# Optimization experiments

Measured on AMD Instinct MI355X. Metric: run time of the kernel, lower is better.

The kernel has to match this reference:

```python
import jax, jax.numpy as jnp
import numpy as np

DIM = 2048
N_HEADS = 16
N_KV_HEADS = 8
HEAD_DIM = DIM // N_HEADS  # 128
N_REP = N_HEADS // N_KV_HEADS
BATCH = 2
SEQ = 2048
CHUNK = 128  # chunked-parallel causal linear attention; SEQ % CHUNK == 0


def _make_freqs_cis(seq_len, head_dim, theta=10000.0):
    freqs = 1.0 / (theta ** (np.arange(0, head_dim, 2, dtype=np.float32) / head_dim))
    t = np.arange(seq_len, dtype=np.float32)
    ang = np.outer(t, freqs)  # [S, D/2]
    return jnp.asarray(np.stack([np.cos(ang), np.sin(ang)], axis=-1))  # [S, D/2, 2]


def setup_inputs() -> dict:
    key = jax.random.key(0)
    ks = jax.random.split(key, 5)
    x = jax.random.normal(ks[0], (BATCH, SEQ, DIM), dtype=jnp.float32)
    freqs_cis = _make_freqs_cis(SEQ, HEAD_DIM)
    s = 0.02
    wq = s * jax.random.normal(ks[1], (N_HEADS * HEAD_DIM, DIM), dtype=jnp.float32)
    wk = s * jax.random.normal(ks[2], (N_KV_HEADS * HEAD_DIM, DIM), dtype=jnp.float32)
    wv = s * jax.random.normal(ks[3], (N_KV_HEADS * HEAD_DIM, DIM), dtype=jnp.float32)
    wo = s * jax.random.normal(ks[4], (DIM, N_HEADS * HEAD_DIM), dtype=jnp.float32)
    return {"x": x, "freqs_cis": freqs_cis, "wq": wq, "wk": wk, "wv": wv, "wo": wo}


def _apply_rotary(x, freqs_cis):
    # x: [B, S, H, D]; freqs_cis: [S, D/2, 2] (cos, sin). Llama pairing: (x0,x1),(x2,x3),...
    B, S, H, D = x.shape
    xr = x.reshape(B, S, H, D // 2, 2)
    x0, x1 = xr[..., 0], xr[..., 1]
    c = freqs_cis[None, :, None, :, 0]
    s = freqs_cis[None, :, None, :, 1]
    o0 = x0 * c - x1 * s
    o1 = x0 * s + x1 * c
    return jnp.stack([o0, o1], axis=-1).reshape(B, S, H, D)


def _causal_linear_attention(q, k, v):
    # q, k, v: [B, H, S, D]; output_i = q_i @ sum_{j<=i} k_j^T v_j
    B, H, S, D = q.shape
    q = jax.nn.softmax(q * (D ** -0.5), axis=-1)  # softmax over feature dim
    k = jax.nn.softmax(k, axis=2)                 # softmax over sequence dim (as in source)
    Nc = S // CHUNK
    qc = q.reshape(B, H, Nc, CHUNK, D)
    kc = k.reshape(B, H, Nc, CHUNK, D)
    vc = v.reshape(B, H, Nc, CHUNK, D)
    # per-chunk KV outer-product sums: [B, H, Nc, D, D]
    kv = jnp.einsum('bhncd,bhnce->bhnde', kc, vc)
    cum = jnp.cumsum(kv, axis=2)
    cum_excl = jnp.concatenate([jnp.zeros_like(cum[:, :, :1]), cum[:, :, :-1]], axis=2)
    inter = jnp.einsum('bhncd,bhnde->bhnce', qc, cum_excl)
    scores = jnp.einsum('bhncd,bhnmd->bhncm', qc, kc)  # [B,H,Nc,C,C]
    mask = jnp.tril(jnp.ones((CHUNK, CHUNK), dtype=bool))
    scores = jnp.where(mask, scores, jnp.zeros((), dtype=scores.dtype))
    intra = jnp.einsum('bhncm,bhnme->bhnce', scores, vc)
    return (inter + intra).reshape(B, H, S, D)


def reference(x, freqs_cis, wq, wk, wv, wo):
    B, S, _ = x.shape
    xq = (x @ wq.T).reshape(B, S, N_HEADS, HEAD_DIM)
    xk = (x @ wk.T).reshape(B, S, N_KV_HEADS, HEAD_DIM)
    xv = (x @ wv.T).reshape(B, S, N_KV_HEADS, HEAD_DIM)
    xq = _apply_rotary(xq, freqs_cis)
    xk = _apply_rotary(xk, freqs_cis)
    # repeat_kv: each kv head repeated N_REP consecutive times
    keys = jnp.repeat(xk, N_REP, axis=2)
    values = jnp.repeat(xv, N_REP, axis=2)
    q = jnp.transpose(xq, (0, 2, 1, 3))
    k = jnp.transpose(keys, (0, 2, 1, 3))
    v = jnp.transpose(values, (0, 2, 1, 3))
    out = _causal_linear_attention(q, k, v)  # [B, H, S, D]
    out = jnp.transpose(out, (0, 2, 1, 3)).reshape(B, S, N_HEADS * HEAD_DIM)
    return out @ wo.T
```

## Files before the change

### kernel.cpp

```cpp
#include <hip/hip_runtime.h>
#include <math.h>

#define DIMV 2048
#define NHEAD 16
#define NKV 8
#define HD 128
#define BATCH 2
#define SEQ 2048
#define CHUNK 128
#define NCHUNK 16
#define MTOK 4096
#define KVD (NKV * HD)

typedef _Float16 half8_t __attribute__((ext_vector_type(8)));
typedef _Float16 half4_t __attribute__((ext_vector_type(4)));
typedef _Float16 half2_t __attribute__((ext_vector_type(2)));
typedef float f32x4 __attribute__((ext_vector_type(4)));

#define GLOBAL_AS __attribute__((address_space(1)))
#define LDS_AS __attribute__((address_space(3)))

__global__ __launch_bounds__(256) void cast_all(const float* __restrict__ x,
                                                const float* __restrict__ wq,
                                                const float* __restrict__ wk,
                                                const float* __restrict__ wv,
                                                const float* __restrict__ wo,
                                                _Float16* __restrict__ xh,
                                                _Float16* __restrict__ wqkvh,
                                                _Float16* __restrict__ woh) {
  long i = (long)(blockIdx.x * 256 + threadIdx.x) * 8;
  const float* src;
  _Float16* dst;
  long off;
  if (i < 8388608)        { src = x;  dst = xh;              off = 0; }
  else if (i < 12582912)  { src = wq; dst = wqkvh;           off = 8388608; }
  else if (i < 14680064)  { src = wk; dst = wqkvh + 4194304; off = 12582912; }
  else if (i < 16777216)  { src = wv; dst = wqkvh + 6291456; off = 14680064; }
  else                    { src = wo; dst = woh;             off = 16777216; }
  long e = i - off;
  float4 a = *(const float4*)&src[e];
  float4 b = *(const float4*)&src[e + 4];
  half8_t h = {(_Float16)a.x, (_Float16)a.y, (_Float16)a.z, (_Float16)a.w,
               (_Float16)b.x, (_Float16)b.y, (_Float16)b.z, (_Float16)b.w};
  *(half8_t*)&dst[e] = h;
}

__global__ __launch_bounds__(256) void transpose_fc(const float* __restrict__ fc,
                                                    float* __restrict__ fcT) {
  __shared__ float T[64][65];
  int s0 = blockIdx.x * 64, d0 = blockIdx.y * 64;
  int t = threadIdx.x;
  int r = t >> 4, c4 = (t & 15) * 4;
#pragma unroll
  for (int p = 0; p < 4; ++p) {
    int sr = p * 16 + r;
    float4 v = *(const float4*)&fc[(size_t)(s0 + sr) * 128 + d0 + c4];
    T[sr][c4] = v.x; T[sr][c4 + 1] = v.y; T[sr][c4 + 2] = v.z; T[sr][c4 + 3] = v.w;
  }
  __syncthreads();
#pragma unroll
  for (int p = 0; p < 4; ++p) {
    int dr = p * 16 + r;
    float4 v = make_float4(T[c4][dr], T[c4 + 1][dr], T[c4 + 2][dr], T[c4 + 3][dr]);
    *(float4*)&fcT[(size_t)(d0 + dr) * SEQ + s0 + c4] = v;
  }
}

#define BARX() __builtin_amdgcn_s_barrier()
#define WAITL0() asm volatile("s_waitcnt lgkmcnt(0)" ::: "memory")
#define WAITVM(n) asm volatile("s_waitcnt vmcnt(" #n ")" ::: "memory")

#define STG_A(bb, kk, i, k0)                                                      \
  __builtin_amdgcn_global_load_lds(                                               \
      (const GLOBAL_AS void*)(A + aoff + (size_t)(i) * 128 * 2048 + (k0) + (kk) * 32), \
      (LDS_AS void*)(As + ((bb) * 2 + (kk)) * 8192 + (i) * 4096 + wave * 512), 16, 0, 0)
#define STG_B(bb, kk, i, k0)                                                      \
  __builtin_amdgcn_global_load_lds(                                               \
      (const GLOBAL_AS void*)(B + boff + (size_t)(i) * 128 * 2048 + (k0) + (kk) * 32), \
      (LDS_AS void*)(Bs + ((bb) * 2 + (kk)) * 8192 + (i) * 4096 + wave * 512), 16, 0, 0)

#define LDA_F(bb, kk, ih) do {                                                    \
    const _Float16* pA_ = As + ((bb) * 2 + (kk)) * 8192 +                         \
                          (wr * 128 + (ih) * 64 + m16) * 32 + pseg8;              \
    af[0] = *(const half8_t*)(pA_);                                               \
    af[1] = *(const half8_t*)(pA_ + 512);                                         \
    af[2] = *(const half8_t*)(pA_ + 1024);                                        \
    af[3] = *(const half8_t*)(pA_ + 1536);                                        \
  } while (0)
#define LDB_F(bb, kk) do {                                                        \
    const _Float16* pB_ = Bs + ((bb) * 2 + (kk)) * 8192 +                         \
                          (wc * 64 + m16) * 32 + pseg8;                           \
    bf[0] = *(const half8_t*)(pB_);                                               \
    bf[1] = *(const half8_t*)(pB_ + 512);                                         \
    bf[2] = *(const half8_t*)(pB_ + 1024);                                        \
    bf[3] = *(const half8_t*)(pB_ + 1536);                                        \
  } while (0)

#define MMX(ih) do {                                                              \
    _Pragma("unroll")                                                             \
    for (int i_ = 0; i_ < 4; ++i_)                                                \
      _Pragma("unroll")                                                           \
      for (int j_ = 0; j_ < 4; ++j_)                                              \
        acc[(ih) * 4 + i_][j_] = __builtin_amdgcn_mfma_f32_16x16x32_f16(          \
            af[i_], bf[j_], acc[(ih) * 4 + i_][j_], 0, 0, 0);                     \
  } while (0)

#define KTILE(bb, k0, DS1, DS2, DS3, DS4, VA, VB) do {                            \
  half8_t af[4], bf[4];                                                           \
                                                           \
  LDA_F(bb, 0, 0); LDB_F(bb, 0);                                                  \
  if (DS1) { STG_A(1 - (bb), 1, 0, (k0) + 64); STG_A(1 - (bb), 1, 1, (k0) + 64); } \
  BARX(); WAITL0();                                                               \
  __builtin_amdgcn_s_setprio(1); MMX(0); __builtin_amdgcn_s_setprio(0);           \
  BARX();                                                                         \
                                                \
  LDA_F(bb, 0, 1);                                                                \
  if (DS2) { STG_B(1 - (bb), 1, 0, (k0) + 64); STG_B(1 - (bb), 1, 1, (k0) + 64); } \
  WAITVM(VA);                                                                     \
  BARX(); WAITL0();                                                               \
  __builtin_amdgcn_s_setprio(1); MMX(1); __builtin_amdgcn_s_setprio(0);           \
  BARX();                                                                         \
                                                           \
  LDA_F(bb, 1, 0); LDB_F(bb, 1);                                                  \
  if (DS3) { STG_A(bb, 0, 0, (k0) + 128); STG_A(bb, 0, 1, (k0) + 128); }          \
  BARX(); WAITL0();                                                               \
  __builtin_amdgcn_s_setprio(1); MMX(0); __builtin_amdgcn_s_setprio(0);           \
  BARX();                                                                         \
                                                \
  LDA_F(bb, 1, 1);                                                                \
  if (DS4) { STG_B(bb, 0, 0, (k0) + 128); STG_B(bb, 0, 1, (k0) + 128); }          \
  WAITVM(VB);                                                                     \
  BARX(); WAITL0();                                                               \
  __builtin_amdgcn_s_setprio(1); MMX(1); __builtin_amdgcn_s_setprio(0);           \
  BARX();                                                                         \
} while (0)

__global__ __launch_bounds__(512, 2) void hgemm_qkv_8p(const _Float16* __restrict__ A,
                                                       const _Float16* __restrict__ B,
                                                       const float* __restrict__ fc,
                                                       _Float16* __restrict__ qh,
                                                       _Float16* __restrict__ kT,
                                                       _Float16* __restrict__ vT) {
  const int K = 2048;
  __shared__ _Float16 As[32768];
  __shared__ _Float16 Bs[32768];
  __shared__ float qsum[4][256];

  const int tid = threadIdx.x;
  const int lane = tid & 63;
  const int wave = tid >> 6;
  const int wr = wave >> 2;
  const int wc = wave & 3;
  const int m16 = lane & 15, quad = lane >> 4;
  const int row0 = blockIdx.y * 256, col0 = blockIdx.x * 256;
  const int pseg8 = (quad ^ ((m16 >> 1) & 3)) * 8;

  const int r_ld = tid >> 2;
  const int sseg = (tid & 3) ^ ((tid >> 3) & 3);
  const size_t aoff = (size_t)(row0 + r_ld) * K + sseg * 8;
  const size_t boff = (size_t)(col0 + r_ld) * K + sseg * 8;

  f32x4 acc[8][4];
#pragma unroll
  for (int m = 0; m < 8; ++m)
#pragma unroll
    for (int j = 0; j < 4; ++j) acc[m][j] = (f32x4){0.f, 0.f, 0.f, 0.f};

  STG_A(0, 0, 0, 0); STG_A(0, 0, 1, 0); STG_B(0, 0, 0, 0); STG_B(0, 0, 1, 0);
  STG_A(0, 1, 0, 0); STG_A(0, 1, 1, 0); STG_B(0, 1, 0, 0); STG_B(0, 1, 1, 0);
  STG_A(1, 0, 0, 64); STG_A(1, 0, 1, 64); STG_B(1, 0, 0, 64); STG_B(1, 0, 1, 64);
  WAITVM(8);
  BARX();

  for (int t = 0; t < 30; t += 2) {
    KTILE(0, t * 64,      1, 1, 1, 1, 8, 8);
    KTILE(1, t * 64 + 64, 1, 1, 1, 1, 8, 8);
  }
  KTILE(0, 1920, 1, 1, 0, 0, 8, 4);
  KTILE(1, 1984, 0, 0, 0, 0, 0, 0);

  if (col0 < 2048) {
    const float sc = 0.08838834764831845f;
    float psum[8][4];
#pragma unroll
    for (int m = 0; m < 8; ++m)
#pragma unroll
      for (int r = 0; r < 4; ++r) psum[m][r] = 0.f;
#pragma unroll
    for (int m = 0; m < 8; ++m)
#pragma unroll
      for (int j = 0; j < 4; ++j) {
        int dl2 = (wc * 64 + j * 16 + m16) & 126;
#pragma unroll
        for (int r = 0; r < 4; ++r) {
          float val = acc[m][j][r];
          float par = __shfl_xor(val, 1);
          int row_l = wr * 128 + (m >> 2) * 64 + (m & 3) * 16 + quad * 4 + r;
          int s_tok = (row0 + row_l) & (SEQ - 1);
          float2 cs = *(const float2*)&fc[(size_t)s_tok * 128 + dl2];
          float o = val * cs.x + par * ((m16 & 1) ? cs.y : -cs.y);
          float e = __expf(o * sc);
          acc[m][j][r] = e;
          psum[m][r] += e;
        }
      }
#pragma unroll
    for (int mm = 1; mm < 16; mm <<= 1)
#pragma unroll
      for (int m = 0; m < 8; ++m)
#pragma unroll
        for (int r = 0; r < 4; ++r) psum[m][r] += __shfl_xor(psum[m][r], mm);
    if (m16 == 0) {
#pragma unroll
      for (int m = 0; m < 8; ++m)
#pragma unroll
        for (int r = 0; r < 4; ++r) {
          int row_l = wr * 128 + (m >> 2) * 64 + (m & 3) * 16 + quad * 4 + r;
          qsum[wc][row_l] = psum[m][r];
        }
    }
    __syncthreads();
#pragma unroll
    for (int m = 0; m < 8; ++m)
#pragma unroll
      for (int r = 0; r < 4; ++r) {
        int row_l = wr * 128 + (m >> 2) * 64 + (m & 3) * 16 + quad * 4 + r;
        psum[m][r] = 1.f / (qsum[wc & 2][row_l] + qsum[(wc & 2) | 1][row_l]);
      }
#pragma unroll
    for (int m = 0; m < 8; ++m)
#pragma unroll
      for (int j = 0; j < 4; ++j) {
        int col = col0 + wc * 64 + j * 16 + m16;
#pragma unroll
        for (int r = 0; r < 4; ++r) {
          int row_l = wr * 128 + (m >> 2) * 64 + (m & 3) * 16 + quad * 4 + r;
          qh[(size_t)(row0 + row_l) * DIMV + col] = (_Float16)(acc[m][j][r] * psum[m][r]);
        }
      }
  } else {
#pragma unroll
    for (int m = 0; m < 8; ++m)
#pragma unroll
      for (int j = 0; j < 4; ++j) {
        int col = col0 + wc * 64 + j * 16 + m16;
        int rowb = row0 + wr * 128 + (m >> 2) * 64 + (m & 3) * 16 + quad * 4;
        half4_t hv = {(_Float16)acc[m][j][0], (_Float16)acc[m][j][1],
                      (_Float16)acc[m][j][2], (_Float16)acc[m][j][3]};
        if (col0 < 3072) {
          *(half4_t*)&kT[(size_t)(col - 2048) * MTOK + rowb] = hv;
        } else {
          *(half4_t*)&vT[(size_t)(col - 3072) * MTOK + rowb] = hv;
        }
      }
  }
}

__global__ __launch_bounds__(256) void hgemm_bt64_f32(const _Float16* __restrict__ A,
                                                      const _Float16* __restrict__ B,
                                                      float* __restrict__ C,
                                                      int M, int N, int K) {
  __shared__ _Float16 As[128 * 64];
  __shared__ _Float16 Bs[128 * 64];
  const int tid = threadIdx.x;
  const int lane = tid & 63;
  const int wave = tid >> 6;
  const int row0 = blockIdx.y * 128, col0 = blockIdx.x * 128;
  const int wr = wave & 1, wc = wave >> 1;
  const int m16 = lane & 15, quad = lane >> 4;

  f32x4 acc[4][4];
#pragma unroll
  for (int i = 0; i < 4; ++i)
#pragma unroll
    for (int j = 0; j < 4; ++j) acc[i][j] = (f32x4){0.f, 0.f, 0.f, 0.f};

  const int r_ld = tid >> 3;
  const int sseg = (tid & 7) ^ (r_ld & 7);
  const size_t a_base = (size_t)(row0 + r_ld) * K + sseg * 8;
  const size_t b_base = (size_t)(col0 + r_ld) * K + sseg * 8;
  _Float16* ldsA = As + wave * 512;
  _Float16* ldsB = Bs + wave * 512;
  const int swzA = quad ^ (m16 & 7);

  for (int k0 = 0; k0 < K; k0 += 64) {
#pragma unroll
    for (int i = 0; i < 4; ++i) {
      __builtin_amdgcn_global_load_lds(
          (const GLOBAL_AS void*)(A + a_base + (size_t)i * 32 * K + k0),
          (LDS_AS void*)(ldsA + i * 2048), 16, 0, 0);
      __builtin_amdgcn_global_load_lds(
          (const GLOBAL_AS void*)(B + b_base + (size_t)i * 32 * K + k0),
          (LDS_AS void*)(ldsB + i * 2048), 16, 0, 0);
    }
    __syncthreads();
#pragma unroll
    for (int kk = 0; kk < 2; ++kk) {
      const int swz = swzA ^ (kk * 4);
      half8_t af[4], bf[4];
#pragma unroll
      for (int i = 0; i < 4; ++i) {
        af[i] = *(half8_t*)&As[(wr * 64 + i * 16 + m16) * 64 + swz * 8];
        bf[i] = *(half8_t*)&Bs[(wc * 64 + i * 16 + m16) * 64 + swz * 8];
      }
#pragma unroll
      for (int i = 0; i < 4; ++i)
#pragma unroll
        for (int j = 0; j < 4; ++j)
          acc[i][j] = __builtin_amdgcn_mfma_f32_16x16x32_f16(af[i], bf[j], acc[i][j], 0, 0, 0);
    }
    __syncthreads();
  }

#pragma unroll
  for (int i = 0; i < 4; ++i)
#pragma unroll
    for (int j = 0; j < 4; ++j) {
      int col = col0 + wc * 64 + j * 16 + m16;
      int rowb = row0 + wr * 64 + i * 16 + quad * 4;
#pragma unroll
      for (int r = 0; r < 4; ++r) C[(size_t)(rowb + r) * N + col] = acc[i][j][r];
    }
}

__global__ __launch_bounds__(256) void k_rope_softmax_T(_Float16* __restrict__ kT,
                                                        const float* __restrict__ fcT) {
  int bi = blockIdx.x;
  int b = bi & 1, pr = bi >> 1;
  int d0 = pr * 2, dl = d0 & 127;
  int t = threadIdx.x;
  size_t r0 = (size_t)d0 * MTOK + b * SEQ + t * 8;
  size_t r1 = r0 + MTOK;
  half8_t x0v = *(half8_t*)&kT[r0];
  half8_t x1v = *(half8_t*)&kT[r1];
  int s8 = t * 8;
  float4 ca = *(const float4*)&fcT[(size_t)dl * SEQ + s8];
  float4 cb = *(const float4*)&fcT[(size_t)dl * SEQ + s8 + 4];
  float4 sa = *(const float4*)&fcT[(size_t)(dl + 1) * SEQ + s8];
  float4 sb = *(const float4*)&fcT[(size_t)(dl + 1) * SEQ + s8 + 4];
  float cc[8] = {ca.x, ca.y, ca.z, ca.w, cb.x, cb.y, cb.z, cb.w};
  float ss[8] = {sa.x, sa.y, sa.z, sa.w, sb.x, sb.y, sb.z, sb.w};
  float e0[8], e1[8];
  float sum0 = 0.f, sum1 = 0.f;
#pragma unroll
  for (int j = 0; j < 8; ++j) {
    float x0 = (float)x0v[j], x1 = (float)x1v[j];
    float o0 = x0 * cc[j] - x1 * ss[j];
    float o1 = x0 * ss[j] + x1 * cc[j];
    e0[j] = expf(o0); e1[j] = expf(o1);
    sum0 += e0[j]; sum1 += e1[j];
  }
#pragma unroll
  for (int off = 1; off < 64; off <<= 1) {
    sum0 += __shfl_xor(sum0, off);
    sum1 += __shfl_xor(sum1, off);
  }
  __shared__ float red[8];
  if ((t & 63) == 0) { red[(t >> 6) * 2] = sum0; red[(t >> 6) * 2 + 1] = sum1; }
  __syncthreads();
  float S0 = red[0] + red[2] + red[4] + red[6];
  float S1 = red[1] + red[3] + red[5] + red[7];
  float i0 = 1.f / S0, i1 = 1.f / S1;
  half8_t w0, w1;
#pragma unroll
  for (int j = 0; j < 8; ++j) {
    w0[j] = (_Float16)(e0[j] * i0);
    w1[j] = (_Float16)(e1[j] * i1);
  }
  *(half8_t*)&kT[r0] = w0;
  *(half8_t*)&kT[r1] = w1;
}

__global__ __launch_bounds__(256) void transpose_k(const _Float16* __restrict__ kT,
                                                   _Float16* __restrict__ kh) {
  __shared__ _Float16 T[64][65];
  int t0 = blockIdx.x * 64, d0 = blockIdx.y * 64;
  int t = threadIdx.x;
  int r = t >> 3, c8 = (t & 7) * 8;
#pragma unroll
  for (int p = 0; p < 2; ++p) {
    int dr = p * 32 + r;
    half8_t v = *(const half8_t*)&kT[(size_t)(d0 + dr) * MTOK + t0 + c8];
#pragma unroll
    for (int j = 0; j < 8; ++j) T[c8 + j][dr] = v[j];
  }
  __syncthreads();
#pragma unroll
  for (int p = 0; p < 2; ++p) {
    int tr = p * 32 + r;
    half8_t v;
#pragma unroll
    for (int j = 0; j < 8; ++j) v[j] = T[tr][c8 + j];
    *(half8_t*)&kh[(size_t)(t0 + tr) * KVD + d0 + c8] = v;
  }
}

__global__ __launch_bounds__(256) void kv_chunk_mfma(const _Float16* __restrict__ vT,
                                                     const _Float16* __restrict__ kT,
                                                     float* __restrict__ kvT) {
  __shared__ _Float16 As[128 * 32];
  __shared__ _Float16 Bs[128 * 32];
  int bi = blockIdx.x;
  int n = bi & 15, kvh = (bi >> 4) & 7, b = bi >> 7;
  int tok0 = b * SEQ + n * CHUNK;
  const int tid = threadIdx.x;
  const int lane = tid & 63;
  const int wave = tid >> 6;
  const int wr = wave & 1, wc = wave >> 1;
  const int m16 = lane & 15, quad = lane >> 4;
  const int qsw8 = (quad ^ ((m16 >> 1) & 3)) * 8;

  f32x4 acc[4][4];
#pragma unroll
  for (int i = 0; i < 4; ++i)
#pragma unroll
    for (int j = 0; j < 4; ++j) acc[i][j] = (f32x4){0.f, 0.f, 0.f, 0.f};

  const int r_ld = tid >> 2;
  const int sseg = (tid & 3) ^ ((tid >> 3) & 3);
  const size_t a_base = (size_t)(kvh * HD + r_ld) * MTOK + tok0 + sseg * 8;
  const size_t b_base = a_base;
  _Float16* ldsA = As + wave * 512;
  _Float16* ldsB = Bs + wave * 512;

  for (int k0 = 0; k0 < 128; k0 += 32) {
#pragma unroll
    for (int i = 0; i < 2; ++i) {
      __builtin_amdgcn_global_load_lds(
          (const GLOBAL_AS void*)(vT + a_base + (size_t)i * 64 * MTOK + k0),
          (LDS_AS void*)(ldsA + i * 2048), 16, 0, 0);
      __builtin_amdgcn_global_load_lds(
          (const GLOBAL_AS void*)(kT + b_base + (size_t)i * 64 * MTOK + k0),
          (LDS_AS void*)(ldsB + i * 2048), 16, 0, 0);
    }
    __syncthreads();
    half8_t af[4], bf[4];
#pragma unroll
    for (int i = 0; i < 4; ++i) {
      af[i] = *(half8_t*)&As[(wr * 64 + i * 16 + m16) * 32 + qsw8];
      bf[i] = *(half8_t*)&Bs[(wc * 64 + i * 16 + m16) * 32 + qsw8];
    }
#pragma unroll
    for (int i = 0; i < 4; ++i)
#pragma unroll
      for (int j = 0; j < 4; ++j)
        acc[i][j] = __builtin_amdgcn_mfma_f32_16x16x32_f16(af[i], bf[j], acc[i][j], 0, 0, 0);
    __syncthreads();
  }
#pragma unroll
  for (int i = 0; i < 4; ++i)
#pragma unroll
    for (int j = 0; j < 4; ++j) {
      int col = wc * 64 + j * 16 + m16;
      int rowb = wr * 64 + i * 16 + quad * 4;
#pragma unroll
      for (int r = 0; r < 4; ++r)
        kvT[(size_t)bi * 16384 + (size_t)(rowb + r) * 128 + col] = acc[i][j][r];
    }
}

__global__ __launch_bounds__(256) void cumsum_h(const float* __restrict__ kvT,
                                                _Float16* __restrict__ cumh) {
  int gid = blockIdx.x * 256 + threadIdx.x;
  int bk = gid >> 14, idx = gid & 16383;
  size_t base = (size_t)bk * NCHUNK * 16384 + idx;
  float run = 0.f;
#pragma unroll
  for (int n = 0; n < NCHUNK; ++n) {
    cumh[base + (size_t)n * 16384] = (_Float16)run;
    run += kvT[base + (size_t)n * 16384];
  }
}

__global__ __launch_bounds__(256) void attn_fused(const _Float16* __restrict__ qh,
                                                  const _Float16* __restrict__ kh,
                                                  const _Float16* __restrict__ cumh,
                                                  const _Float16* __restrict__ vT,
                                                  _Float16* __restrict__ ath) {
  __shared__ _Float16 As[128 * 32];
  __shared__ _Float16 Bs[128 * 32];
  __shared__ _Float16 Ss[128][136];
  int bi = blockIdx.x;
  int n = bi & 15, h = (bi >> 4) & 15, b = bi >> 8;
  int kvh = h >> 1;
  int tok0 = b * SEQ + n * CHUNK;
  const int tid = threadIdx.x;
  const int lane = tid & 63;
  const int wave = tid >> 6;
  const int wr = wave & 1, wc = wave >> 1;
  const int m16 = lane & 15, quad = lane >> 4;
  const int qsw8 = (quad ^ ((m16 >> 1) & 3)) * 8;
  const int r_ld = tid >> 2;
  const int sseg = (tid & 3) ^ ((tid >> 3) & 3);
  _Float16* ldsA = As + wave * 512;
  _Float16* ldsB = Bs + wave * 512;

  f32x4 acc[4][4];
#pragma unroll
  for (int i = 0; i < 4; ++i)
#pragma unroll
    for (int j = 0; j < 4; ++j) acc[i][j] = (f32x4){0.f, 0.f, 0.f, 0.f};

  const size_t qbase = (size_t)(tok0 + r_ld) * DIMV + h * HD + sseg * 8;
  const size_t kbase = (size_t)(tok0 + r_ld) * KVD + kvh * HD + sseg * 8;
  const size_t cbase = ((size_t)((b * 8 + kvh) * 16 + n)) * 16384 + (size_t)r_ld * 128 + sseg * 8;
  const size_t vbase = (size_t)(kvh * HD + r_ld) * MTOK + tok0 + sseg * 8;

  for (int k0 = 0; k0 < 128; k0 += 32) {
#pragma unroll
    for (int i = 0; i < 2; ++i) {
      __builtin_amdgcn_global_load_lds(
          (const GLOBAL_AS void*)(qh + qbase + (size_t)i * 64 * DIMV + k0),
          (LDS_AS void*)(ldsA + i * 2048), 16, 0, 0);
      __builtin_amdgcn_global_load_lds(
          (const GLOBAL_AS void*)(kh + kbase + (size_t)i * 64 * KVD + k0),
          (LDS_AS void*)(ldsB + i * 2048), 16, 0, 0);
    }
    __syncthreads();
    half8_t af[4], bf[4];
#pragma unroll
    for (int i = 0; i < 4; ++i) {
      af[i] = *(half8_t*)&As[(wr * 64 + i * 16 + m16) * 32 + qsw8];
      bf[i] = *(half8_t*)&Bs[(wc * 64 + i * 16 + m16) * 32 + qsw8];
    }
#pragma unroll
    for (int i = 0; i < 4; ++i)
#pragma unroll
      for (int j = 0; j < 4; ++j)
        acc[i][j] = __builtin_amdgcn_mfma_f32_16x16x32_f16(af[i], bf[j], acc[i][j], 0, 0, 0);
    __syncthreads();
  }

#pragma unroll
  for (int i = 0; i < 4; ++i)
#pragma unroll
    for (int j = 0; j < 4; ++j) {
      int col = wc * 64 + j * 16 + m16;
      int rowb = wr * 64 + i * 16 + quad * 4;
#pragma unroll
      for (int r = 0; r < 4; ++r) {
        float v = (col <= rowb + r) ? acc[i][j][r] : 0.f;
        Ss[rowb + r][col] = (_Float16)v;
      }
      acc[i][j] = (f32x4){0.f, 0.f, 0.f, 0.f};
    }

  for (int ks = 0; ks < 4; ++ks) {
    int k0 = ks * 32;
#pragma unroll
    for (int i = 0; i < 2; ++i) {
      __builtin_amdgcn_global_load_lds(
          (const GLOBAL_AS void*)(qh + qbase + (size_t)i * 64 * DIMV + k0),
          (LDS_AS void*)(ldsA + i * 2048), 16, 0, 0);
      __builtin_amdgcn_global_load_lds(
          (const GLOBAL_AS void*)(cumh + cbase + (size_t)i * 64 * 128 + k0),
          (LDS_AS void*)(ldsB + i * 2048), 16, 0, 0);
    }
    __syncthreads();
    half8_t af[4], bf[4];
#pragma unroll
    for (int i = 0; i < 4; ++i) {
      af[i] = *(half8_t*)&As[(wr * 64 + i * 16 + m16) * 32 + qsw8];
      bf[i] = *(half8_t*)&Bs[(wc * 64 + i * 16 + m16) * 32 + qsw8];
    }
#pragma unroll
    for (int i = 0; i < 4; ++i)
#pragma unroll
      for (int j = 0; j < 4; ++j)
        acc[i][j] = __builtin_amdgcn_mfma_f32_16x16x32_f16(af[i], bf[j], acc[i][j], 0, 0, 0);
    __syncthreads();
  }

  for (int ks = 0; ks < 4; ++ks) {
    int k0 = ks * 32;
#pragma unroll
    for (int i = 0; i < 2; ++i) {
      __builtin_amdgcn_global_load_lds(
          (const GLOBAL_AS void*)(vT + vbase + (size_t)i * 64 * MTOK + k0),
          (LDS_AS void*)(ldsB + i * 2048), 16, 0, 0);
    }
    __syncthreads();
    half8_t af[4], bf[4];
#pragma unroll
    for (int i = 0; i < 4; ++i) {
      af[i] = *(half8_t*)&Ss[wr * 64 + i * 16 + m16][k0 + quad * 8];
      bf[i] = *(half8_t*)&Bs[(wc * 64 + i * 16 + m16) * 32 + qsw8];
    }
#pragma unroll
    for (int i = 0; i < 4; ++i)
#pragma unroll
      for (int j = 0; j < 4; ++j)
        acc[i][j] = __builtin_amdgcn_mfma_f32_16x16x32_f16(af[i], bf[j], acc[i][j], 0, 0, 0);
    __syncthreads();
  }

#pragma unroll
  for (int i = 0; i < 4; ++i)
#pragma unroll
    for (int j = 0; j < 4; ++j) {
      int col = wc * 64 + j * 16 + m16;
      int rowb = wr * 64 + i * 16 + quad * 4;
#pragma unroll
      for (int r = 0; r < 4; ++r)
        ath[(size_t)(tok0 + rowb + r) * DIMV + h * HD + col] = (_Float16)acc[i][j][r];
    }
}

extern "C" void kernel_launch(void* const* d_in, const int* in_sizes, int n_in,
                              void* d_out, int out_size, void* d_ws, size_t ws_size,
                              hipStream_t stream) {
  const float* x  = (const float*)d_in[0];
  const float* fc = (const float*)d_in[1];
  const float* wq = (const float*)d_in[2];
  const float* wk = (const float*)d_in[3];
  const float* wv = (const float*)d_in[4];
  const float* wo = (const float*)d_in[5];
  float* out = (float*)d_out;

  char* p = (char*)d_ws;
  _Float16* xh    = (_Float16*)p;  p += 16777216;
  _Float16* wqkvh = (_Float16*)p;  p += 16777216;
  _Float16* woh   = (_Float16*)p;  p += 8388608;
  _Float16* qh    = (_Float16*)p;  p += 16777216;
  _Float16* kT    = (_Float16*)p;  p += 8388608;
  _Float16* kh    = (_Float16*)p;  p += 8388608;
  _Float16* vT    = (_Float16*)p;  p += 8388608;
  float*    kvT   = (float*)p;     p += 16777216;
  _Float16* cumh  = (_Float16*)p;  p += 8388608;
  _Float16* ath   = (_Float16*)p;  p += 16777216;
  float*    fcT   = (float*)p;     p += 1048576;

  cast_all<<<10240, 256, 0, stream>>>(x, wq, wk, wv, wo, xh, wqkvh, woh);
  transpose_fc<<<dim3(32, 2), 256, 0, stream>>>(fc, fcT);

  hgemm_qkv_8p<<<dim3(16, 16), 512, 0, stream>>>(xh, wqkvh, fc, qh, kT, vT);

  k_rope_softmax_T<<<1024, 256, 0, stream>>>(kT, fcT);
  transpose_k<<<dim3(64, 16), 256, 0, stream>>>(kT, kh);

  kv_chunk_mfma<<<256, 256, 0, stream>>>(vT, kT, kvT);
  cumsum_h<<<1024, 256, 0, stream>>>(kvT, cumh);
  attn_fused<<<512, 256, 0, stream>>>(qh, kh, cumh, vT, ath);

  hgemm_bt64_f32<<<dim3(16, 32), 256, 0, stream>>>(ath, woh, out, MTOK, 2048, 2048);
}
```

Before: 290.0 us.

## Software-pipeline LDS fragment reads across MFMA phases in QKV GEMM

```diff
diff --git a/kernel.cpp b/kernel.cpp
--- a/kernel.cpp
+++ b/kernel.cpp
@@ -67,8 +67,15 @@
 }
 
 #define BARX() __builtin_amdgcn_s_barrier()
-#define WAITL0() asm volatile("s_waitcnt lgkmcnt(0)" ::: "memory")
+#define SBAR0() __builtin_amdgcn_sched_barrier(0)
+#define PRIO1() __builtin_amdgcn_s_setprio(1)
+#define PRIO0() __builtin_amdgcn_s_setprio(0)
+#define WAITL(n) asm volatile("s_waitcnt lgkmcnt(" #n ")" ::: "memory")
 #define WAITVM(n) asm volatile("s_waitcnt vmcnt(" #n ")" ::: "memory")
+
+__device__ __forceinline__ unsigned lds_addr(const void* p) {
+  return (unsigned)(size_t)(const LDS_AS void*)p;
+}
 
 #define STG_A(bb, kk, i, k0)                                                      \
   __builtin_amdgcn_global_load_lds(                                               \
@@ -79,60 +86,59 @@
       (const GLOBAL_AS void*)(B + boff + (size_t)(i) * 128 * 2048 + (k0) + (kk) * 32), \
       (LDS_AS void*)(Bs + ((bb) * 2 + (kk)) * 8192 + (i) * 4096 + wave * 512), 16, 0, 0)
 
-#define LDA_F(bb, kk, ih) do {                                                    \
-    const _Float16* pA_ = As + ((bb) * 2 + (kk)) * 8192 +                         \
-                          (wr * 128 + (ih) * 64 + m16) * 32 + pseg8;              \
-    af[0] = *(const half8_t*)(pA_);                                               \
-    af[1] = *(const half8_t*)(pA_ + 512);                                         \
-    af[2] = *(const half8_t*)(pA_ + 1024);                                        \
-    af[3] = *(const half8_t*)(pA_ + 1536);                                        \
-  } while (0)
-#define LDB_F(bb, kk) do {                                                        \
-    const _Float16* pB_ = Bs + ((bb) * 2 + (kk)) * 8192 +                         \
-                          (wc * 64 + m16) * 32 + pseg8;                           \
-    bf[0] = *(const half8_t*)(pB_);                                               \
-    bf[1] = *(const half8_t*)(pB_ + 512);                                         \
-    bf[2] = *(const half8_t*)(pB_ + 1024);                                        \
-    bf[3] = *(const half8_t*)(pB_ + 1536);                                        \
-  } while (0)
-
-#define MMX(ih) do {                                                              \
+#define RD_A(dst, bb, kk, ih, i)                                                  \
+  asm volatile("ds_read_b128 %0, %1" : "=v"(dst)                                  \
+               : "v"(lds_addr(Abase_p + ((bb) * 2 + (kk)) * 8192 +                \
+                              ((ih) * 64 + (i) * 16) * 32)))
+#define RD_B(dst, bb, kk, i)                                                      \
+  asm volatile("ds_read_b128 %0, %1" : "=v"(dst)                                  \
+               : "v"(lds_addr(Bbase_p + ((bb) * 2 + (kk)) * 8192 + (i) * 16 * 32)))
+
+#define MM16(aa, bbf, ih) do {                                                    \
     _Pragma("unroll")                                                             \
     for (int i_ = 0; i_ < 4; ++i_)                                                \
       _Pragma("unroll")                                                           \
       for (int j_ = 0; j_ < 4; ++j_)                                              \
         acc[(ih) * 4 + i_][j_] = __builtin_amdgcn_mfma_f32_16x16x32_f16(          \
-            af[i_], bf[j_], acc[(ih) * 4 + i_][j_], 0, 0, 0);                     \
+            (aa)[i_], (bbf)[j_], acc[(ih) * 4 + i_][j_], 0, 0, 0);                \
   } while (0)
 
-#define KTILE(bb, k0, DS1, DS2, DS3, DS4, VA, VB) do {                            \
-  half8_t af[4], bf[4];                                                           \
-                                                           \
-  LDA_F(bb, 0, 0); LDB_F(bb, 0);                                                  \
+#define KTILE2(bb, k0, DS1, DS2, DS3, DS4, VA, VB, PF) do {                       \
+                                                                          \
+  RD_A(A1f[0], bb, 0, 1, 0); RD_A(A1f[1], bb, 0, 1, 1);                           \
+  RD_A(A1f[2], bb, 0, 1, 2); RD_A(A1f[3], bb, 0, 1, 3);                           \
   if (DS1) { STG_A(1 - (bb), 1, 0, (k0) + 64); STG_A(1 - (bb), 1, 1, (k0) + 64); } \
-  BARX(); WAITL0();                                                               \
-  __builtin_amdgcn_s_setprio(1); MMX(0); __builtin_amdgcn_s_setprio(0);           \
-  BARX();                                                                         \
-                                                \
-  LDA_F(bb, 0, 1);                                                                \
+  WAITL(4); SBAR0(); BARX();                                                      \
+  PRIO1(); MM16(A0f, BXf, 0); PRIO0(); BARX();                                    \
+                                                                          \
   if (DS2) { STG_B(1 - (bb), 1, 0, (k0) + 64); STG_B(1 - (bb), 1, 1, (k0) + 64); } \
-  WAITVM(VA);                                                                     \
-  BARX(); WAITL0();                                                               \
-  __builtin_amdgcn_s_setprio(1); MMX(1); __builtin_amdgcn_s_setprio(0);           \
-  BARX();                                                                         \
-                                                           \
-  LDA_F(bb, 1, 0); LDB_F(bb, 1);                                                  \
+  WAITVM(VA); BARX(); SBAR0();                                                    \
+  RD_A(A0f[0], bb, 1, 0, 0); RD_A(A0f[1], bb, 1, 0, 1);                           \
+  RD_A(A0f[2], bb, 1, 0, 2); RD_A(A0f[3], bb, 1, 0, 3);                           \
+  RD_B(BYf[0], bb, 1, 0); RD_B(BYf[1], bb, 1, 1);                                 \
+  RD_B(BYf[2], bb, 1, 2); RD_B(BYf[3], bb, 1, 3);                                 \
+  WAITL(8); SBAR0();                                                              \
+  PRIO1(); MM16(A1f, BXf, 1); PRIO0(); BARX();                                    \
+                                                                          \
+  RD_A(A1f[0], bb, 1, 1, 0); RD_A(A1f[1], bb, 1, 1, 1);                           \
+  RD_A(A1f[2], bb, 1, 1, 2); RD_A(A1f[3], bb, 1, 1, 3);                           \
   if (DS3) { STG_A(bb, 0, 0, (k0) + 128); STG_A(bb, 0, 1, (k0) + 128); }          \
-  BARX(); WAITL0();                                                               \
-  __builtin_amdgcn_s_setprio(1); MMX(0); __builtin_amdgcn_s_setprio(0);           \
-  BARX();                                                                         \
-                                                \
-  LDA_F(bb, 1, 1);                                                                \
+  WAITL(4); SBAR0(); BARX();                                                      \
+  PRIO1(); MM16(A0f, BYf, 0); PRIO0(); BARX();                                    \
+                                                                          \
   if (DS4) { STG_B(bb, 0, 0, (k0) + 128); STG_B(bb, 0, 1, (k0) + 128); }          \
-  WAITVM(VB);                                                                     \
-  BARX(); WAITL0();                                                               \
-  __builtin_amdgcn_s_setprio(1); MMX(1); __builtin_amdgcn_s_setprio(0);           \
-  BARX();                                                                         \
+  WAITVM(VB); BARX(); SBAR0();                                                    \
+  if (PF) {                                                                       \
+    RD_A(A0f[0], 1 - (bb), 0, 0, 0); RD_A(A0f[1], 1 - (bb), 0, 0, 1);             \
+    RD_A(A0f[2], 1 - (bb), 0, 0, 2); RD_A(A0f[3], 1 - (bb), 0, 0, 3);             \
+    RD_B(BXf[0], 1 - (bb), 0, 0); RD_B(BXf[1], 1 - (bb), 0, 1);                   \
+    RD_B(BXf[2], 1 - (bb), 0, 2); RD_B(BXf[3], 1 - (bb), 0, 3);                   \
+    WAITL(8);                                                                     \
+  } else {                                                                        \
+    WAITL(0);                                                                     \
+  }                                                                               \
+  SBAR0();                                                                        \
+  PRIO1(); MM16(A1f, BYf, 1); PRIO0(); BARX();                                    \
 } while (0)
 
 __global__ __launch_bounds__(512, 2) void hgemm_qkv_8p(const _Float16* __restrict__ A,
@@ -155,6 +161,9 @@
   const int row0 = blockIdx.y * 256, col0 = blockIdx.x * 256;
   const int pseg8 = (quad ^ ((m16 >> 1) & 3)) * 8;
 
+  const _Float16* Abase_p = As + (wr * 128 + m16) * 32 + pseg8;
+  const _Float16* Bbase_p = Bs + (wc * 64 + m16) * 32 + pseg8;
+
   const int r_ld = tid >> 2;
   const int sseg = (tid & 3) ^ ((tid >> 3) & 3);
   const size_t aoff = (size_t)(row0 + r_ld) * K + sseg * 8;
@@ -166,18 +175,24 @@
 #pragma unroll
     for (int j = 0; j < 4; ++j) acc[m][j] = (f32x4){0.f, 0.f, 0.f, 0.f};
 
+  half8_t A0f[4], A1f[4], BXf[4], BYf[4];
+
   STG_A(0, 0, 0, 0); STG_A(0, 0, 1, 0); STG_B(0, 0, 0, 0); STG_B(0, 0, 1, 0);
   STG_A(0, 1, 0, 0); STG_A(0, 1, 1, 0); STG_B(0, 1, 0, 0); STG_B(0, 1, 1, 0);
   STG_A(1, 0, 0, 64); STG_A(1, 0, 1, 64); STG_B(1, 0, 0, 64); STG_B(1, 0, 1, 64);
   WAITVM(8);
-  BARX();
+  BARX(); SBAR0();
+  RD_A(A0f[0], 0, 0, 0, 0); RD_A(A0f[1], 0, 0, 0, 1);
+  RD_A(A0f[2], 0, 0, 0, 2); RD_A(A0f[3], 0, 0, 0, 3);
+  RD_B(BXf[0], 0, 0, 0); RD_B(BXf[1], 0, 0, 1);
+  RD_B(BXf[2], 0, 0, 2); RD_B(BXf[3], 0, 0, 3);
 
   for (int t = 0; t < 30; t += 2) {
-    KTILE(0, t * 64,      1, 1, 1, 1, 8, 8);
-    KTILE(1, t * 64 + 64, 1, 1, 1, 1, 8, 8);
-  }
-  KTILE(0, 1920, 1, 1, 0, 0, 8, 4);
-  KTILE(1, 1984, 0, 0, 0, 0, 0, 0);
+    KTILE2(0, t * 64,      1, 1, 1, 1, 8, 8, 1);
+    KTILE2(1, t * 64 + 64, 1, 1, 1, 1, 8, 8, 1);
+  }
+  KTILE2(0, 1920, 1, 1, 0, 0, 8, 4, 1);
+  KTILE2(1, 1984, 0, 0, 0, 0, 0, 0, 0);
 
   if (col0 < 2048) {
     const float sc = 0.08838834764831845f;
```

Measured after the change: 303.2 us. +4.6%, slower.

## Double-buffer LDS staging in KV-chunk and chunk-attention kernels, keep Q resident

Applied to the files above, without the earlier changes.

```diff
diff --git a/kernel.cpp b/kernel.cpp
--- a/kernel.cpp
+++ b/kernel.cpp
@@ -19,6 +19,10 @@
 
 #define GLOBAL_AS __attribute__((address_space(1)))
 #define LDS_AS __attribute__((address_space(3)))
+
+#define BARX() __builtin_amdgcn_s_barrier()
+#define WAITL(n) asm volatile("s_waitcnt lgkmcnt(" #n ")" ::: "memory")
+#define WAITVM(n) asm volatile("s_waitcnt vmcnt(" #n ")" ::: "memory")
 
 __global__ __launch_bounds__(256) void cast_all(const float* __restrict__ x,
                                                 const float* __restrict__ wq,
@@ -66,10 +70,6 @@
   }
 }
 
-#define BARX() __builtin_amdgcn_s_barrier()
-#define WAITL0() asm volatile("s_waitcnt lgkmcnt(0)" ::: "memory")
-#define WAITVM(n) asm volatile("s_waitcnt vmcnt(" #n ")" ::: "memory")
-
 #define STG_A(bb, kk, i, k0)                                                      \
   __builtin_amdgcn_global_load_lds(                                               \
       (const GLOBAL_AS void*)(A + aoff + (size_t)(i) * 128 * 2048 + (k0) + (kk) * 32), \
@@ -110,27 +110,27 @@
                                                            \
   LDA_F(bb, 0, 0); LDB_F(bb, 0);                                                  \
   if (DS1) { STG_A(1 - (bb), 1, 0, (k0) + 64); STG_A(1 - (bb), 1, 1, (k0) + 64); } \
-  BARX(); WAITL0();                                                               \
+  BARX(); WAITL(0);                                                               \
   __builtin_amdgcn_s_setprio(1); MMX(0); __builtin_amdgcn_s_setprio(0);           \
   BARX();                                                                         \
                                                 \
   LDA_F(bb, 0, 1);                                                                \
   if (DS2) { STG_B(1 - (bb), 1, 0, (k0) + 64); STG_B(1 - (bb), 1, 1, (k0) + 64); } \
   WAITVM(VA);                                                                     \
-  BARX(); WAITL0();                                                               \
+  BARX(); WAITL(0);                                                               \
   __builtin_amdgcn_s_setprio(1); MMX(1); __builtin_amdgcn_s_setprio(0);           \
   BARX();                                                                         \
                                                            \
   LDA_F(bb, 1, 0); LDB_F(bb, 1);                                                  \
   if (DS3) { STG_A(bb, 0, 0, (k0) + 128); STG_A(bb, 0, 1, (k0) + 128); }          \
-  BARX(); WAITL0();                                                               \
+  BARX(); WAITL(0);                                                               \
   __builtin_amdgcn_s_setprio(1); MMX(0); __builtin_amdgcn_s_setprio(0);           \
   BARX();                                                                         \
                                                 \
   LDA_F(bb, 1, 1);                                                                \
   if (DS4) { STG_B(bb, 0, 0, (k0) + 128); STG_B(bb, 0, 1, (k0) + 128); }          \
   WAITVM(VB);                                                                     \
-  BARX(); WAITL0();                                                               \
+  BARX(); WAITL(0);                                                               \
   __builtin_amdgcn_s_setprio(1); MMX(1); __builtin_amdgcn_s_setprio(0);           \
   BARX();                                                                         \
 } while (0)
@@ -398,8 +398,8 @@
 __global__ __launch_bounds__(256) void kv_chunk_mfma(const _Float16* __restrict__ vT,
                                                      const _Float16* __restrict__ kT,
                                                      float* __restrict__ kvT) {
-  __shared__ _Float16 As[128 * 32];
-  __shared__ _Float16 Bs[128 * 32];
+  __shared__ _Float16 As[2][128 * 32];
+  __shared__ _Float16 Bs[2][128 * 32];
   int bi = blockIdx.x;
   int n = bi & 15, kvh = (bi >> 4) & 7, b = bi >> 7;
   int tok0 = b * SEQ + n * CHUNK;
@@ -419,33 +419,47 @@
   const int r_ld = tid >> 2;
   const int sseg = (tid & 3) ^ ((tid >> 3) & 3);
   const size_t a_base = (size_t)(kvh * HD + r_ld) * MTOK + tok0 + sseg * 8;
-  const size_t b_base = a_base;
-  _Float16* ldsA = As + wave * 512;
-  _Float16* ldsB = Bs + wave * 512;
-
-  for (int k0 = 0; k0 < 128; k0 += 32) {
-#pragma unroll
-    for (int i = 0; i < 2; ++i) {
-      __builtin_amdgcn_global_load_lds(
-          (const GLOBAL_AS void*)(vT + a_base + (size_t)i * 64 * MTOK + k0),
-          (LDS_AS void*)(ldsA + i * 2048), 16, 0, 0);
-      __builtin_amdgcn_global_load_lds(
-          (const GLOBAL_AS void*)(kT + b_base + (size_t)i * 64 * MTOK + k0),
-          (LDS_AS void*)(ldsB + i * 2048), 16, 0, 0);
-    }
-    __syncthreads();
+
+#pragma unroll
+  for (int i = 0; i < 2; ++i) {
+    __builtin_amdgcn_global_load_lds(
+        (const GLOBAL_AS void*)(vT + a_base + (size_t)i * 64 * MTOK),
+        (LDS_AS void*)(&As[0][0] + i * 2048 + wave * 512), 16, 0, 0);
+    __builtin_amdgcn_global_load_lds(
+        (const GLOBAL_AS void*)(kT + a_base + (size_t)i * 64 * MTOK),
+        (LDS_AS void*)(&Bs[0][0] + i * 2048 + wave * 512), 16, 0, 0);
+  }
+
+#pragma unroll
+  for (int s = 0; s < 4; ++s) {
+    WAITVM(0);
+    BARX();
+    if (s < 3) {
+      const int k0 = (s + 1) * 32;
+      const int bb = (s + 1) & 1;
+#pragma unroll
+      for (int i = 0; i < 2; ++i) {
+        __builtin_amdgcn_global_load_lds(
+            (const GLOBAL_AS void*)(vT + a_base + (size_t)i * 64 * MTOK + k0),
+            (LDS_AS void*)(&As[bb][0] + i * 2048 + wave * 512), 16, 0, 0);
+        __builtin_amdgcn_global_load_lds(
+            (const GLOBAL_AS void*)(kT + a_base + (size_t)i * 64 * MTOK + k0),
+            (LDS_AS void*)(&Bs[bb][0] + i * 2048 + wave * 512), 16, 0, 0);
+      }
+    }
+    const _Float16* ra = &As[s & 1][0];
+    const _Float16* rb = &Bs[s & 1][0];
     half8_t af[4], bf[4];
 #pragma unroll
     for (int i = 0; i < 4; ++i) {
-      af[i] = *(half8_t*)&As[(wr * 64 + i * 16 + m16) * 32 + qsw8];
-      bf[i] = *(half8_t*)&Bs[(wc * 64 + i * 16 + m16) * 32 + qsw8];
+      af[i] = *(const half8_t*)&ra[(wr * 64 + i * 16 + m16) * 32 + qsw8];
+      bf[i] = *(const half8_t*)&rb[(wc * 64 + i * 16 + m16) * 32 + qsw8];
     }
 #pragma unroll
     for (int i = 0; i < 4; ++i)
 #pragma unroll
       for (int j = 0; j < 4; ++j)
         acc[i][j] = __builtin_amdgcn_mfma_f32_16x16x32_f16(af[i], bf[j], acc[i][j], 0, 0, 0);
-    __syncthreads();
   }
 #pragma unroll
   for (int i = 0; i < 4; ++i)
@@ -477,9 +491,9 @@
                                                   const _Float16* __restrict__ cumh,
                                                   const _Float16* __restrict__ vT,
                                                   _Float16* __restrict__ ath) {
-  __shared__ _Float16 As[128 * 32];
-  __shared__ _Float16 Bs[128 * 32];
-  __shared__ _Float16 Ss[128][136];
+  __shared__ _Float16 Qs[128 * 128];
+  __shared__ _Float16 Bs[2][128 * 32];
+  __shared__ _Float16 Ss[128 * 128];
   int bi = blockIdx.x;
   int n = bi & 15, h = (bi >> 4) & 15, b = bi >> 8;
   int kvh = h >> 1;
@@ -492,8 +506,6 @@
   const int qsw8 = (quad ^ ((m16 >> 1) & 3)) * 8;
   const int r_ld = tid >> 2;
   const int sseg = (tid & 3) ^ ((tid >> 3) & 3);
-  _Float16* ldsA = As + wave * 512;
-  _Float16* ldsB = Bs + wave * 512;
 
   f32x4 acc[4][4];
 #pragma unroll
@@ -501,97 +513,98 @@
 #pragma unroll
     for (int j = 0; j < 4; ++j) acc[i][j] = (f32x4){0.f, 0.f, 0.f, 0.f};
 
-  const size_t qbase = (size_t)(tok0 + r_ld) * DIMV + h * HD + sseg * 8;
+  const int qrow = tid >> 4;
+  const int qsl = (tid & 15) ^ (qrow & 7);
+  const size_t qsrc = (size_t)(tok0 + qrow) * DIMV + h * HD + qsl * 8;
+#pragma unroll
+  for (int p = 0; p < 8; ++p)
+    __builtin_amdgcn_global_load_lds(
+        (const GLOBAL_AS void*)(qh + qsrc + (size_t)p * 16 * DIMV),
+        (LDS_AS void*)(Qs + p * 2048 + wave * 512), 16, 0, 0);
+
   const size_t kbase = (size_t)(tok0 + r_ld) * KVD + kvh * HD + sseg * 8;
   const size_t cbase = ((size_t)((b * 8 + kvh) * 16 + n)) * 16384 + (size_t)r_ld * 128 + sseg * 8;
   const size_t vbase = (size_t)(kvh * HD + r_ld) * MTOK + tok0 + sseg * 8;
 
-  for (int k0 = 0; k0 < 128; k0 += 32) {
-#pragma unroll
-    for (int i = 0; i < 2; ++i) {
-      __builtin_amdgcn_global_load_lds(
-          (const GLOBAL_AS void*)(qh + qbase + (size_t)i * 64 * DIMV + k0),
-          (LDS_AS void*)(ldsA + i * 2048), 16, 0, 0);
-      __builtin_amdgcn_global_load_lds(
-          (const GLOBAL_AS void*)(kh + kbase + (size_t)i * 64 * KVD + k0),
-          (LDS_AS void*)(ldsB + i * 2048), 16, 0, 0);
-    }
-    __syncthreads();
+#pragma unroll
+  for (int i = 0; i < 2; ++i)
+    __builtin_amdgcn_global_load_lds(
+        (const GLOBAL_AS void*)(kh + kbase + (size_t)i * 64 * KVD),
+        (LDS_AS void*)(&Bs[0][0] + i * 2048 + wave * 512), 16, 0, 0);
+
+#pragma unroll
+  for (int s = 0; s < 12; ++s) {
+    WAITVM(0);
+    BARX();
+    if (s < 11) {
+      const int sn = s + 1;
+      _Float16* dstB = &Bs[sn & 1][0];
+      if (sn < 4) {
+        const int k0 = sn * 32;
+#pragma unroll
+        for (int i = 0; i < 2; ++i)
+          __builtin_amdgcn_global_load_lds(
+              (const GLOBAL_AS void*)(kh + kbase + (size_t)i * 64 * KVD + k0),
+              (LDS_AS void*)(dstB + i * 2048 + wave * 512), 16, 0, 0);
+      } else if (sn < 8) {
+        const int k0 = (sn - 4) * 32;
+#pragma unroll
+        for (int i = 0; i < 2; ++i)
+          __builtin_amdgcn_global_load_lds(
+              (const GLOBAL_AS void*)(cumh + cbase + (size_t)i * 64 * 128 + k0),
+              (LDS_AS void*)(dstB + i * 2048 + wave * 512), 16, 0, 0);
+      } else {
+        const int k0 = (sn - 8) * 32;
+#pragma unroll
+        for (int i = 0; i < 2; ++i)
+          __builtin_amdgcn_global_load_lds(
+              (const GLOBAL_AS void*)(vT + vbase + (size_t)i * 64 * MTOK + k0),
+              (LDS_AS void*)(dstB + i * 2048 + wave * 512), 16, 0, 0);
+      }
+    }
     half8_t af[4], bf[4];
-#pragma unroll
-    for (int i = 0; i < 4; ++i) {
-      af[i] = *(half8_t*)&As[(wr * 64 + i * 16 + m16) * 32 + qsw8];
-      bf[i] = *(half8_t*)&Bs[(wc * 64 + i * 16 + m16) * 32 + qsw8];
+    const _Float16* rb = &Bs[s & 1][0];
+#pragma unroll
+    for (int i = 0; i < 4; ++i)
+      bf[i] = *(const half8_t*)&rb[(wc * 64 + i * 16 + m16) * 32 + qsw8];
+    if (s < 8) {
+      const int sl4 = (s & 3) * 4;
+#pragma unroll
+      for (int i = 0; i < 4; ++i) {
+        int row = wr * 64 + i * 16 + m16;
+        af[i] = *(const half8_t*)&Qs[row * 128 + ((sl4 + quad) ^ (m16 & 7)) * 8];
+      }
+    } else {
+      const int sl4 = (s - 8) * 4;
+#pragma unroll
+      for (int i = 0; i < 4; ++i) {
+        int row = wr * 64 + i * 16 + m16;
+        af[i] = *(const half8_t*)&Ss[row * 128 + ((sl4 + quad) ^ (m16 & 7)) * 8];
+      }
     }
 #pragma unroll
     for (int i = 0; i < 4; ++i)
 #pragma unroll
       for (int j = 0; j < 4; ++j)
         acc[i][j] = __builtin_amdgcn_mfma_f32_16x16x32_f16(af[i], bf[j], acc[i][j], 0, 0, 0);
-    __syncthreads();
-  }
-
-#pragma unroll
-  for (int i = 0; i < 4; ++i)
-#pragma unroll
-    for (int j = 0; j < 4; ++j) {
-      int col = wc * 64 + j * 16 + m16;
-      int rowb = wr * 64 + i * 16 + quad * 4;
-#pragma unroll
-      for (int r = 0; r < 4; ++r) {
-        float v = (col <= rowb + r) ? acc[i][j][r] : 0.f;
-        Ss[rowb + r][col] = (_Float16)v;
-      }
-      acc[i][j] = (f32x4){0.f, 0.f, 0.f, 0.f};
-    }
-
-  for (int ks = 0; ks < 4; ++ks) {
-    int k0 = ks * 32;
-#pragma unroll
-    for (int i = 0; i < 2; ++i) {
-      __builtin_amdgcn_global_load_lds(
-          (const GLOBAL_AS void*)(qh + qbase + (size_t)i * 64 * DIMV + k0),
-          (LDS_AS void*)(ldsA + i * 2048), 16, 0, 0);
-      __builtin_amdgcn_global_load_lds(
-          (const GLOBAL_AS void*)(cumh + cbase + (size_t)i * 64 * 128 + k0),
-          (LDS_AS void*)(ldsB + i * 2048), 16, 0, 0);
-    }
-    __syncthreads();
-    half8_t af[4], bf[4];
-#pragma unroll
-    for (int i = 0; i < 4; ++i) {
-      af[i] = *(half8_t*)&As[(wr * 64 + i * 16 + m16) * 32 + qsw8];
-      bf[i] = *(half8_t*)&Bs[(wc * 64 + i * 16 + m16) * 32 + qsw8];
-    }
-#pragma unroll
-    for (int i = 0; i < 4; ++i)
-#pragma unroll
-      for (int j = 0; j < 4; ++j)
-        acc[i][j] = __builtin_amdgcn_mfma_f32_16x16x32_f16(af[i], bf[j], acc[i][j], 0, 0, 0);
-    __syncthreads();
-  }
-
-  for (int ks = 0; ks < 4; ++ks) {
-    int k0 = ks * 32;
-#pragma unroll
-    for (int i = 0; i < 2; ++i) {
-      __builtin_amdgcn_global_load_lds(
-          (const GLOBAL_AS void*)(vT + vbase + (size_t)i * 64 * MTOK + k0),
-          (LDS_AS void*)(ldsB + i * 2048), 16, 0, 0);
-    }
-    __syncthreads();
-    half8_t af[4], bf[4];
-#pragma unroll
-    for (int i = 0; i < 4; ++i) {
-      af[i] = *(half8_t*)&Ss[wr * 64 + i * 16 + m16][k0 + quad * 8];
-      bf[i] = *(half8_t*)&Bs[(wc * 64 + i * 16 + m16) * 32 + qsw8];
-    }
-#pragma unroll
-    for (int i = 0; i < 4; ++i)
-#pragma unroll
-      for (int j = 0; j < 4; ++j)
-        acc[i][j] = __builtin_amdgcn_mfma_f32_16x16x32_f16(af[i], bf[j], acc[i][j], 0, 0, 0);
-    __syncthreads();
+    if (s == 3) {
+#pragma unroll
+      for (int i = 0; i < 4; ++i)
+#pragma unroll
+        for (int j = 0; j < 4; ++j) {
+          int col = wc * 64 + j * 16 + m16;
+          int rowb = wr * 64 + i * 16 + quad * 4;
+#pragma unroll
+          for (int r = 0; r < 4; ++r) {
+            int row = rowb + r;
+            float v = (col <= row) ? acc[i][j][r] : 0.f;
+            int sp = (col >> 3) ^ (row & 7);
+            Ss[row * 128 + sp * 8 + (col & 7)] = (_Float16)v;
+          }
+          acc[i][j] = (f32x4){0.f, 0.f, 0.f, 0.f};
+        }
+      WAITL(0);
+    }
   }
 
 #pragma unroll
```

Result: no change. 294.9 us (+1.7%).
